# Kernel tuning notes

Measured on AMD Instinct MI355X. Metric: run time of the kernel, lower is better.

## Reference

```python
import jax, jax.numpy as jnp
import numpy as np

N_EMBED = 256
N_HEAD = 8
HEAD = N_EMBED // N_HEAD
LN_EPS = 1e-5


def _layernorm(x, g, b):
    mu = jnp.mean(x, axis=-1, keepdims=True)
    var = jnp.mean(jnp.square(x - mu), axis=-1, keepdims=True)
    return (x - mu) * jax.lax.rsqrt(var + LN_EPS) * g + b


def setup_inputs() -> dict:
    key = jax.random.key(0)
    ks = jax.random.split(key, 12)
    B, T, C, H, D = 16, 1024, N_EMBED, N_HEAD, HEAD
    s = C ** -0.5
    return {
        "x": jax.random.normal(ks[0], (B, T, C), jnp.float32),
        "wq": jax.random.normal(ks[1], (H, C, D), jnp.float32) * s,
        "wk": jax.random.normal(ks[2], (H, C, D), jnp.float32) * s,
        "wv": jax.random.normal(ks[3], (H, C, D), jnp.float32) * s,
        "w_proj": jax.random.normal(ks[4], (C, C), jnp.float32) * s,
        "b_proj": jnp.zeros((C,), jnp.float32),
        "w1": jax.random.normal(ks[5], (C, 4 * C), jnp.float32) * s,
        "b1": jnp.zeros((4 * C,), jnp.float32),
        "w2": jax.random.normal(ks[6], (4 * C, C), jnp.float32) * (4 * C) ** -0.5,
        "b2": jnp.zeros((C,), jnp.float32),
        "ln1_g": jnp.ones((C,), jnp.float32),
        "ln1_b": jnp.zeros((C,), jnp.float32),
        "ln2_g": jnp.ones((C,), jnp.float32),
        "ln2_b": jnp.zeros((C,), jnp.float32),
    }


def reference(x, wq, wk, wv, w_proj, b_proj, w1, b1, w2, b2,
              ln1_g, ln1_b, ln2_g, ln2_b):
    B, T, C = x.shape
    # --- multi-head causal self-attention on ln1(x) ---
    h = _layernorm(x, ln1_g, ln1_b)
    q = jnp.einsum('btc,hcd->bhtd', h, wq)
    k = jnp.einsum('btc,hcd->bhtd', h, wk)
    v = jnp.einsum('btc,hcd->bhtd', h, wv)
    # NOTE: original scales by n_embed**-0.5 (C of input), not head_size
    wei = jnp.einsum('bhtd,bhsd->bhts', q, k) * (C ** -0.5)
    causal = jnp.tril(jnp.ones((T, T), bool))
    wei = jnp.where(causal, wei, -jnp.inf)
    wei = jax.nn.softmax(wei, axis=-1)
    att = jnp.einsum('bhts,bhsd->bhtd', wei, v)
    att = att.transpose(0, 2, 1, 3).reshape(B, T, C)  # concat heads
    x = x + att @ w_proj + b_proj
    # --- feedforward on ln2(x) ---
    h2 = _layernorm(x, ln2_g, ln2_b)
    f = jax.nn.relu(h2 @ w1 + b1) @ w2 + b2
    return x + f
```

## Files before the change

### kernel.cpp

```cpp
#include <hip/hip_runtime.h>


typedef unsigned short u16;
typedef unsigned int u32;
typedef __attribute__((ext_vector_type(8))) short short8v;
typedef __attribute__((ext_vector_type(4))) float float4v;

__device__ __forceinline__ float b2f(u16 u) { union { u32 i; float f; } v; v.i = (u32)u << 16; return v.f; }
__device__ __forceinline__ float lo2f(u32 u) { union { u32 i; float f; } v; v.i = u << 16; return v.f; }
__device__ __forceinline__ float hi2f(u32 u) { union { u32 i; float f; } v; v.i = u & 0xffff0000u; return v.f; }
__device__ __forceinline__ u16 f2b(float f) {
    union { float f; u32 i; } v; v.f = f;
    u32 r = v.i + 0x7fffu + ((v.i >> 16) & 1u);
    return (u16)(r >> 16);
}
__device__ __forceinline__ u32 pk2_rtz(float a, float b) {
    return (__float_as_uint(a) >> 16) | (__float_as_uint(b) & 0xffff0000u);
}
__device__ __forceinline__ void async_cp16(const u16* g, u16* l) {
    __builtin_amdgcn_global_load_lds((const __attribute__((address_space(1))) void*)g,
                                     (__attribute__((address_space(3))) void*)l, 16, 0, 0);
}

__global__ __launch_bounds__(256) void prep_ln1(const float* __restrict__ wq,
                                                const float* __restrict__ wk,
                                                const float* __restrict__ wv,
                                                const float* __restrict__ wp,
                                                const float* __restrict__ w1,
                                                const float* __restrict__ w2,
                                                const float* __restrict__ x,
                                                const float* __restrict__ g1,
                                                const float* __restrict__ be1,
                                                u16* __restrict__ wqkvT,
                                                u16* __restrict__ wpT,
                                                u16* __restrict__ w1T,
                                                u16* __restrict__ w2T,
                                                u16* __restrict__ hout) {
    __shared__ u16 tile[64][65];
    int bid = blockIdx.x, tid = threadIdx.x;
    if (bid < 768) {
        int i = bid * 256 + tid;
        int n = i >> 8, k = i & 255;
        int which = n >> 8, nn = n & 255;
        const float* w = which == 0 ? wq : (which == 1 ? wk : wv);
        float v = w[((nn >> 5) * 256 + k) * 32 + (nn & 31)];
        if (which == 0) v *= 0.09016844f;
        wqkvT[i] = f2b(v);
    } else if (bid < 912) {
        const float* src; u16* dst; int K, N, t;
        if (bid < 784)      { src = wp; dst = wpT; K = 256;  N = 256;  t = bid - 768; }
        else if (bid < 848) { src = w1; dst = w1T; K = 256;  N = 1024; t = bid - 784; }
        else                { src = w2; dst = w2T; K = 1024; N = 256;  t = bid - 848; }
        int ntn = N >> 6;
        int k0 = (t / ntn) << 6, n0 = (t % ntn) << 6;
        int lane = tid & 63, wrow = tid >> 6;
        #pragma unroll
        for (int r = 0; r < 16; r++) {
            int k = wrow * 16 + r;
            tile[k][lane] = f2b(src[(size_t)(k0 + k) * N + n0 + lane]);
        }
        __syncthreads();
        #pragma unroll
        for (int r = 0; r < 16; r++) {
            int n = wrow * 16 + r;
            dst[(size_t)(n0 + n) * K + k0 + lane] = tile[lane][n];
        }
    } else {
        int row = (bid - 912) * 4 + (tid >> 6);
        int lane = tid & 63;
        float4 xv = *(const float4*)(x + (size_t)row * 256 + lane * 4);
        float v0 = xv.x, v1 = xv.y, v2 = xv.z, v3 = xv.w;
        float s = v0 + v1 + v2 + v3;
        #pragma unroll
        for (int m = 32; m; m >>= 1) s += __shfl_xor(s, m);
        float mu = s * 0.00390625f;
        float d0 = v0 - mu, d1 = v1 - mu, d2 = v2 - mu, d3 = v3 - mu;
        float ss = d0 * d0 + d1 * d1 + d2 * d2 + d3 * d3;
        #pragma unroll
        for (int m = 32; m; m >>= 1) ss += __shfl_xor(ss, m);
        float rs = rsqrtf(ss * 0.00390625f + 1e-5f);
        float4 g = *(const float4*)(g1 + lane * 4);
        float4 b = *(const float4*)(be1 + lane * 4);
        uint2 r;
        r.x = (u32)f2b(d0 * rs * g.x + b.x) | ((u32)f2b(d1 * rs * g.y + b.y) << 16);
        r.y = (u32)f2b(d2 * rs * g.z + b.z) | ((u32)f2b(d3 * rs * g.w + b.w) << 16);
        *(uint2*)(hout + (size_t)row * 256 + lane * 4) = r;
    }
}

template<bool HASBIAS, bool RELU, bool QKV>
__global__ __launch_bounds__(256) void gemm128(const u16* __restrict__ A,
                                               const u16* __restrict__ Bt,
                                               const float* __restrict__ bias,
                                               u16* __restrict__ out,
                                               u16* __restrict__ vout,
                                               int M, int N, int K) {
    __shared__ __align__(16) u16 SH[17408];
    u16* As = SH;
    u16* Bs = SH + 128 * 64;
    const int tid = threadIdx.x, lane = tid & 63, w = tid >> 6;
    const int m0 = blockIdx.x * 128, n0 = blockIdx.y * 128;
    const int wm = (w & 1) * 64, wn = (w >> 1) * 64;
    const int fm = lane & 15, q = lane >> 4;

    float4v acc[4][4];
    #pragma unroll
    for (int i = 0; i < 4; i++)
        #pragma unroll
        for (int j = 0; j < 4; j++) acc[i][j] = (float4v){0.f, 0.f, 0.f, 0.f};

    const int kset = ((lane & 7) ^ (lane >> 3)) * 8;
    const u16* Ag = A  + (size_t)(m0 + w * 32 + (lane >> 3)) * K + kset;
    const u16* Bg = Bt + (size_t)(n0 + w * 32 + (lane >> 3)) * K + kset;
    u16* Asw = As + (w * 32) * 64;
    u16* Bsw = Bs + (w * 32) * 64;

    const int sw = fm & 7;
    for (int k0 = 0; k0 < K; k0 += 64) {
        __syncthreads();
        #pragma unroll
        for (int c = 0; c < 4; c++) {
            async_cp16(Ag + (size_t)c * 8 * K + k0, Asw + c * 8 * 64);
            async_cp16(Bg + (size_t)c * 8 * K + k0, Bsw + c * 8 * 64);
        }
        __syncthreads();
        #pragma unroll
        for (int kk = 0; kk < 64; kk += 32) {
            const int slot = (((kk >> 3) + q) ^ sw) * 8;
            short8v af[4], bf[4];
            #pragma unroll
            for (int mi = 0; mi < 4; mi++)
                af[mi] = *(const short8v*)&As[(wm + mi * 16 + fm) * 64 + slot];
            #pragma unroll
            for (int ni = 0; ni < 4; ni++)
                bf[ni] = *(const short8v*)&Bs[(wn + ni * 16 + fm) * 64 + slot];
            #pragma unroll
            for (int mi = 0; mi < 4; mi++)
                #pragma unroll
                for (int ni = 0; ni < 4; ni++)
                    acc[mi][ni] = __builtin_amdgcn_mfma_f32_16x16x32_bf16(
                        bf[ni], af[mi], acc[mi][ni], 0, 0, 0);
        }
    }

    if (QKV && n0 >= 512) {
        __syncthreads();
        #pragma unroll
        for (int mi = 0; mi < 4; mi++) {
            int ml = wm + mi * 16 + fm;
            #pragma unroll
            for (int ni = 0; ni < 4; ni++) {
                int nl = wn + ni * 16 + q * 4;
                #pragma unroll
                for (int r = 0; r < 4; r++)
                    SH[(nl + r) * 136 + ml] = f2b(acc[mi][ni][r]);
            }
        }
        __syncthreads();
        int r = tid & 127, c = (tid >> 7) << 6;
        int hd = (n0 - 512) + r;
        int b = m0 >> 10, t0 = m0 & 1023;
        u16* dst = vout + (size_t)(b * 256 + hd) * 1024 + t0 + c;
        const u16* srcT = SH + r * 136 + c;
        #pragma unroll
        for (int i = 0; i < 8; i++)
            *(uint4*)(dst + i * 8) = *(const uint4*)(srcT + i * 8);
        return;
    }

    #pragma unroll
    for (int mi = 0; mi < 4; mi++) {
        int row = m0 + wm + mi * 16 + fm;
        #pragma unroll
        for (int ni = 0; ni < 4; ni++) {
            int nb = n0 + wn + ni * 16 + q * 4;
            float v0 = acc[mi][ni][0], v1 = acc[mi][ni][1],
                  v2 = acc[mi][ni][2], v3 = acc[mi][ni][3];
            if (HASBIAS) {
                float4 bv = *(const float4*)&bias[nb];
                v0 += bv.x; v1 += bv.y; v2 += bv.z; v3 += bv.w;
            }
            if (RELU) {
                v0 = fmaxf(v0, 0.f); v1 = fmaxf(v1, 0.f);
                v2 = fmaxf(v2, 0.f); v3 = fmaxf(v3, 0.f);
            }
            size_t idx = (size_t)row * N + nb;
            uint2 ov;
            ov.x = (u32)f2b(v0) | ((u32)f2b(v1) << 16);
            ov.y = (u32)f2b(v2) | ((u32)f2b(v3) << 16);
            *(uint2*)&out[idx] = ov;
        }
    }
}

#define FFN_COMPUTE(ABASE, BBASE, ACC)                                            \
    _Pragma("unroll")                                                             \
    for (int kk = 0; kk < 64; kk += 32) {                                         \
        const int slot = (((kk >> 3) + q) ^ sw) * 8;                              \
        short8v af[2], bf[4];                                                     \
        _Pragma("unroll")                                                         \
        for (int mi = 0; mi < 2; mi++)                                            \
            af[mi] = *(const short8v*)&(ABASE)[(wm + mi * 16 + fm) * 64 + slot];  \
        _Pragma("unroll")                                                         \
        for (int ni = 0; ni < 4; ni++)                                            \
            bf[ni] = *(const short8v*)&(BBASE)[(wn + ni * 16 + fm) * 64 + slot];  \
        _Pragma("unroll")                                                         \
        for (int mi = 0; mi < 2; mi++)                                            \
            _Pragma("unroll")                                                     \
            for (int ni = 0; ni < 4; ni++)                                        \
                ACC[mi][ni] = __builtin_amdgcn_mfma_f32_16x16x32_bf16(            \
                    bf[ni], af[mi], ACC[mi][ni], 0, 0, 0);                        \
    }

__global__ __launch_bounds__(512, 2) void ffn_fused(const u16* __restrict__ h2,
                                                    const u16* __restrict__ w1T,
                                                    const float* __restrict__ b1,
                                                    const u16* __restrict__ w2T,
                                                    const float* __restrict__ b2,
                                                    const u16* __restrict__ x2b,
                                                    float* __restrict__ out) {
    __shared__ __align__(16) u16 SH[65536];
    u16* As = SH;
    u16* Ms = SH + 16384;
    u16* Bs = SH + 32768;
    const int tid = threadIdx.x, lane = tid & 63, w = tid >> 6;
    const int m0 = blockIdx.x * 64;
    const int wm = (w & 1) * 32;
    const int wn = (w >> 1) * 64;
    const int fm = lane & 15, q = lane >> 4;
    const int sw = fm & 7;
    const int kset = ((lane & 7) ^ (lane >> 3)) * 8;
    const int rb = w * 8 + (lane >> 3);

    auto issueB = [&](int t, u16* dst) {
        const int n2 = t >> 3, k2 = t & 3;
        if (((t >> 2) & 1) == 0) {
            const u16* src = w1T + (size_t)(n2 * 256 + rb) * 256 + k2 * 64 + kset;
            #pragma unroll
            for (int c = 0; c < 4; c++)
                async_cp16(src + (size_t)c * 64 * 256, dst + c * 4096);
        } else {
            const u16* src = w2T + (size_t)rb * 1024 + n2 * 256 + k2 * 64 + kset;
            #pragma unroll
            for (int c = 0; c < 4; c++)
                async_cp16(src + (size_t)c * 64 * 1024, dst + c * 4096);
        }
    };

    const u16* Ag = h2 + (size_t)(m0 + rb) * 256 + kset;
    #pragma unroll
    for (int kc = 0; kc < 4; kc++)
        async_cp16(Ag + kc * 64, As + kc * 4096 + w * 512);
    issueB(0, Bs + w * 512);
    issueB(1, Bs + 16384 + w * 512);

    float4v acc1[2][4], acc2[2][4];
    #pragma unroll
    for (int i = 0; i < 2; i++)
        #pragma unroll
        for (int j = 0; j < 4; j++) acc2[i][j] = (float4v){0.f, 0.f, 0.f, 0.f};

    #pragma unroll 1
    for (int t = 0; t < 32; ++t) {
        const int nch = t >> 3, ph = (t >> 2) & 1, kc = t & 3;
        if (t == 31) asm volatile("s_waitcnt vmcnt(0)" ::: "memory");
        else         asm volatile("s_waitcnt vmcnt(4)" ::: "memory");
        __builtin_amdgcn_s_barrier();
        const u16* Bb = Bs + (t & 1) * 16384;
        if (ph == 0) {
            if (kc == 0) {
                #pragma unroll
                for (int i = 0; i < 2; i++)
                    #pragma unroll
                    for (int j = 0; j < 4; j++) acc1[i][j] = (float4v){0.f, 0.f, 0.f, 0.f};
            }
            const u16* Ab = As + kc * 4096;
            FFN_COMPUTE(Ab, Bb, acc1);
            if (kc == 3) {
                #pragma unroll
                for (int ni = 0; ni < 4; ni++) {
                    const int c2 = wn + ni * 16 + q * 4;
                    const int kcM = c2 >> 6, cc = c2 & 63;
                    float4 bv = *(const float4*)&b1[nch * 256 + c2];
                    #pragma unroll
                    for (int mi = 0; mi < 2; mi++) {
                        const int row = wm + mi * 16 + fm;
                        float v0 = fmaxf(acc1[mi][ni][0] + bv.x, 0.f);
                        float v1 = fmaxf(acc1[mi][ni][1] + bv.y, 0.f);
                        float v2 = fmaxf(acc1[mi][ni][2] + bv.z, 0.f);
                        float v3 = fmaxf(acc1[mi][ni][3] + bv.w, 0.f);
                        uint2 pp;
                        pp.x = (u32)f2b(v0) | ((u32)f2b(v1) << 16);
                        pp.y = (u32)f2b(v2) | ((u32)f2b(v3) << 16);
                        *(uint2*)&Ms[kcM * 4096 + row * 64 +
                                     (((cc >> 3) ^ (row & 7)) * 8) + (cc & 7)] = pp;
                    }
                }
            }
        } else {
            const u16* Ab = Ms + kc * 4096;
            FFN_COMPUTE(Ab, Bb, acc2);
        }
        asm volatile("s_waitcnt lgkmcnt(0)" ::: "memory");
        __builtin_amdgcn_s_barrier();
        if (t + 2 < 32)
            issueB(t + 2, Bs + (t & 1) * 16384 + w * 512);
    }

    #pragma unroll
    for (int mi = 0; mi < 2; mi++) {
        const int row = m0 + wm + mi * 16 + fm;
        #pragma unroll
        for (int ni = 0; ni < 4; ni++) {
            const int nb = wn + ni * 16 + q * 4;
            size_t idx = (size_t)row * 256 + nb;
            float4 bv = *(const float4*)&b2[nb];
            uint2 rv = *(const uint2*)&x2b[idx];
            float v0 = acc2[mi][ni][0] + bv.x + lo2f(rv.x);
            float v1 = acc2[mi][ni][1] + bv.y + hi2f(rv.x);
            float v2 = acc2[mi][ni][2] + bv.z + lo2f(rv.y);
            float v3 = acc2[mi][ni][3] + bv.w + hi2f(rv.y);
            *(float4*)&out[idx] = (float4){v0, v1, v2, v3};
        }
    }
}

__global__ __launch_bounds__(256) void proj_ln2(const u16* __restrict__ att,
                                                const u16* __restrict__ wpT,
                                                const float* __restrict__ bp,
                                                const float* __restrict__ x,
                                                const float* __restrict__ g2,
                                                const float* __restrict__ be2,
                                                u16* __restrict__ x2b,
                                                u16* __restrict__ h2) {
    __shared__ __align__(16) u16 As[32 * 64];
    __shared__ __align__(16) u16 Bs[256 * 64];
    __shared__ float gs[256], bs[256], bps[256];
    __shared__ float ps[4][16], pq[4][16];
    const int tid = threadIdx.x, lane = tid & 63, w = tid >> 6;
    const int m0 = blockIdx.x * 32;
    const int wm = (w & 1) * 16, wn = (w >> 1) * 128;
    const int fm = lane & 15, q = lane >> 4;

    gs[tid] = g2[tid]; bs[tid] = be2[tid]; bps[tid] = bp[tid];

    float4v acc[8];
    #pragma unroll
    for (int i = 0; i < 8; i++) acc[i] = (float4v){0.f, 0.f, 0.f, 0.f};

    const int kset = ((lane & 7) ^ (lane >> 3)) * 8;
    const u16* Ag = att + (size_t)(m0 + w * 8 + (lane >> 3)) * 256 + kset;
    const u16* Bg = wpT + (size_t)(w * 64 + (lane >> 3)) * 256 + kset;
    u16* Asw = As + (w * 8) * 64;
    u16* Bsw = Bs + (w * 64) * 64;

    const int sw = fm & 7;
    for (int k0 = 0; k0 < 256; k0 += 64) {
        __syncthreads();
        async_cp16(Ag + k0, Asw);
        #pragma unroll
        for (int c = 0; c < 8; c++)
            async_cp16(Bg + (size_t)c * 8 * 256 + k0, Bsw + c * 8 * 64);
        __syncthreads();
        #pragma unroll
        for (int kk = 0; kk < 64; kk += 32) {
            const int slot = (((kk >> 3) + q) ^ sw) * 8;
            short8v af = *(const short8v*)&As[(wm + fm) * 64 + slot];
            #pragma unroll
            for (int ni = 0; ni < 8; ni++) {
                short8v bf = *(const short8v*)&Bs[(wn + ni * 16 + fm) * 64 + slot];
                acc[ni] = __builtin_amdgcn_mfma_f32_16x16x32_bf16(bf, af, acc[ni], 0, 0, 0);
            }
        }
    }

    int m = m0 + wm + fm;
    float v[8][4];
    float s = 0.f, sq = 0.f;
    #pragma unroll
    for (int ni = 0; ni < 8; ni++) {
        int nb = wn + ni * 16 + q * 4;
        float4 xv = *(const float4*)(x + (size_t)m * 256 + nb);
        float4 bv = *(const float4*)&bps[nb];
        #pragma unroll
        for (int r = 0; r < 4; r++) {
            float t = acc[ni][r] + (&bv.x)[r] + (&xv.x)[r];
            v[ni][r] = t;
            s += t; sq += t * t;
        }
    }
    s += __shfl_xor(s, 16);  s += __shfl_xor(s, 32);
    sq += __shfl_xor(sq, 16); sq += __shfl_xor(sq, 32);
    if (q == 0) { ps[w][fm] = s; pq[w][fm] = sq; }
    __syncthreads();
    s = ps[w][fm] + ps[w ^ 2][fm];
    sq = pq[w][fm] + pq[w ^ 2][fm];
    float mu = s * 0.00390625f;
    float rs = rsqrtf(sq * 0.00390625f - mu * mu + 1e-5f);
    #pragma unroll
    for (int ni = 0; ni < 8; ni++) {
        int nb = wn + ni * 16 + q * 4;
        size_t idx = (size_t)m * 256 + nb;
        float4 gv = *(const float4*)&gs[nb];
        float4 bv = *(const float4*)&bs[nb];
        uint2 xo, ho;
        xo.x = (u32)f2b(v[ni][0]) | ((u32)f2b(v[ni][1]) << 16);
        xo.y = (u32)f2b(v[ni][2]) | ((u32)f2b(v[ni][3]) << 16);
        float h0 = (v[ni][0] - mu) * rs * gv.x + bv.x;
        float h1 = (v[ni][1] - mu) * rs * gv.y + bv.y;
        float h2v = (v[ni][2] - mu) * rs * gv.z + bv.z;
        float h3 = (v[ni][3] - mu) * rs * gv.w + bv.w;
        ho.x = (u32)f2b(h0) | ((u32)f2b(h1) << 16);
        ho.y = (u32)f2b(h2v) | ((u32)f2b(h3) << 16);
        *(uint2*)&x2b[idx] = xo;
        *(uint2*)&h2[idx] = ho;
    }
}

__global__ __launch_bounds__(256) void attn_mfma(const u16* __restrict__ qk,
                                                 const u16* __restrict__ vtg,
                                                 u16* __restrict__ att) {
    const int T = 1024;
    int jj = (blockIdx.x + (blockIdx.y >> 3)) & 7;
    int b = blockIdx.y >> 3, hh = blockIdx.y & 7;
    int tid = threadIdx.x;
    int lane = tid & 63, w = tid >> 6;
    int fm = lane & 15, q = lane >> 4;

    __shared__ __align__(16) u16 Ks[64][72];
    __shared__ __align__(16) u16 Vt[32][72];
    __shared__ __align__(16) u16 Pl[4][16][72];

    size_t base = (size_t)b * T * 512;
    const u16* kb = qk + base + 256 + hh * 32;
    const u16* vt = vtg + (size_t)((b * 8 + hh) * 32) * 1024;
    const int krow = tid >> 2, kcol = (tid & 3) * 8;
    const int vd = tid >> 3, vs = (tid & 7) * 8;

    int qa0 = jj * 64, qb0 = (15 - jj) * 64;
    int tqa = qa0 + w * 16 + fm, tqb = qb0 + w * 16 + fm;
    short8v qfa = *(const short8v*)(qk + base + (size_t)tqa * 512 + hh * 32 + q * 8);
    short8v qfb = *(const short8v*)(qk + base + (size_t)tqb * 512 + hh * 32 + q * 8);
    float4v oa0 = {0.f, 0.f, 0.f, 0.f}, oa1 = {0.f, 0.f, 0.f, 0.f};
    float4v ob0 = {0.f, 0.f, 0.f, 0.f}, ob1 = {0.f, 0.f, 0.f, 0.f};
    float la = 0.f, lb = 0.f;
    int wqa = qa0 + w * 16, wqb = qb0 + w * 16;
    int nIter = 16 - jj;

    uint4 kreg = *(const uint4*)(kb + (size_t)krow * 512 + kcol);
    uint4 vreg = *(const uint4*)(vt + (size_t)vd * 1024 + vs);

    for (int it = 0; it < nIter; ++it) {
        int s0 = it << 6;
        __syncthreads();
        *(uint4*)&Ks[krow][kcol] = kreg;
        *(uint4*)&Vt[vd][vs] = vreg;
        __syncthreads();
        if (it + 1 < nIter) {
            int ns0 = s0 + 64;
            kreg = *(const uint4*)(kb + (size_t)(ns0 + krow) * 512 + kcol);
            vreg = *(const uint4*)(vt + (size_t)vd * 1024 + ns0 + vs);
        }
        short8v kf0 = *(const short8v*)&Ks[fm][q * 8];
        short8v kf1 = *(const short8v*)&Ks[16 + fm][q * 8];
        short8v kf2 = *(const short8v*)&Ks[32 + fm][q * 8];
        short8v kf3 = *(const short8v*)&Ks[48 + fm][q * 8];
        short8v vf00 = *(const short8v*)&Vt[fm][q * 8];
        short8v vf01 = *(const short8v*)&Vt[fm][32 + q * 8];
        short8v vf10 = *(const short8v*)&Vt[16 + fm][q * 8];
        short8v vf11 = *(const short8v*)&Vt[16 + fm][32 + q * 8];
        float4v z = {0.f, 0.f, 0.f, 0.f};

        #pragma unroll
        for (int t2 = 0; t2 < 2; t2++) {
            int wq0 = t2 ? wqa : wqb;
            if (s0 >= wq0 + 16) continue;
            int tq = t2 ? tqa : tqb;
            short8v qf = t2 ? qfa : qfb;
            float4v s_0 = __builtin_amdgcn_mfma_f32_16x16x32_bf16(kf0, qf, z, 0, 0, 0);
            float4v s_1 = __builtin_amdgcn_mfma_f32_16x16x32_bf16(kf1, qf, z, 0, 0, 0);
            float4v s_2 = __builtin_amdgcn_mfma_f32_16x16x32_bf16(kf2, qf, z, 0, 0, 0);
            float4v s_3 = __builtin_amdgcn_mfma_f32_16x16x32_bf16(kf3, qf, z, 0, 0, 0);
            float p[16];
            #pragma unroll
            for (int r = 0; r < 4; r++) {
                p[r] = exp2f(s_0[r]); p[4 + r] = exp2f(s_1[r]);
                p[8 + r] = exp2f(s_2[r]); p[12 + r] = exp2f(s_3[r]);
            }
            if (s0 + 63 > wq0) {
                int sb = s0 + q * 4;
                #pragma unroll
                for (int c = 0; c < 4; c++)
                    #pragma unroll
                    for (int r = 0; r < 4; r++)
                        if (sb + c * 16 + r > tq) p[c * 4 + r] = 0.f;
            }
            float rsum = 0.f;
            #pragma unroll
            for (int i = 0; i < 16; i++) rsum += p[i];
            rsum += __shfl_xor(rsum, 16);
            rsum += __shfl_xor(rsum, 32);
            if (t2) la += rsum; else lb += rsum;

            #pragma unroll
            for (int c = 0; c < 4; c++) {
                uint2 pp;
                pp.x = pk2_rtz(p[c * 4 + 0], p[c * 4 + 1]);
                pp.y = pk2_rtz(p[c * 4 + 2], p[c * 4 + 3]);
                *(uint2*)&Pl[w][fm][c * 16 + q * 4] = pp;
            }
            short8v pf0 = *(const short8v*)&Pl[w][fm][q * 8];
            short8v pf1 = *(const short8v*)&Pl[w][fm][32 + q * 8];
            if (t2) {
                oa0 = __builtin_amdgcn_mfma_f32_16x16x32_bf16(vf00, pf0, oa0, 0, 0, 0);
                oa0 = __builtin_amdgcn_mfma_f32_16x16x32_bf16(vf01, pf1, oa0, 0, 0, 0);
                oa1 = __builtin_amdgcn_mfma_f32_16x16x32_bf16(vf10, pf0, oa1, 0, 0, 0);
                oa1 = __builtin_amdgcn_mfma_f32_16x16x32_bf16(vf11, pf1, oa1, 0, 0, 0);
            } else {
                ob0 = __builtin_amdgcn_mfma_f32_16x16x32_bf16(vf00, pf0, ob0, 0, 0, 0);
                ob0 = __builtin_amdgcn_mfma_f32_16x16x32_bf16(vf01, pf1, ob0, 0, 0, 0);
                ob1 = __builtin_amdgcn_mfma_f32_16x16x32_bf16(vf10, pf0, ob1, 0, 0, 0);
                ob1 = __builtin_amdgcn_mfma_f32_16x16x32_bf16(vf11, pf1, ob1, 0, 0, 0);
            }
        }
    }

    #pragma unroll
    for (int t2 = 0; t2 < 2; t2++) {
        float inv = 1.f / (t2 ? la : lb);
        float4v o0 = t2 ? oa0 : ob0, o1 = t2 ? oa1 : ob1;
        int tq = t2 ? tqa : tqb;
        uint2 r0, r1;
        r0.x = (u32)f2b(o0[0] * inv) | ((u32)f2b(o0[1] * inv) << 16);
        r0.y = (u32)f2b(o0[2] * inv) | ((u32)f2b(o0[3] * inv) << 16);
        r1.x = (u32)f2b(o1[0] * inv) | ((u32)f2b(o1[1] * inv) << 16);
        r1.y = (u32)f2b(o1[2] * inv) | ((u32)f2b(o1[3] * inv) << 16);
        size_t o = (size_t)(b * T + tq) * 256 + hh * 32;
        *(uint2*)(att + o + q * 4) = r0;
        *(uint2*)(att + o + 16 + q * 4) = r1;
    }
}

extern "C" void kernel_launch(void* const* d_in, const int* in_sizes, int n_in,
                              void* d_out, int out_size, void* d_ws, size_t ws_size,
                              hipStream_t stream) {
    const int BT = 16 * 1024;
    const float* x      = (const float*)d_in[0];
    const float* wq     = (const float*)d_in[1];
    const float* wk     = (const float*)d_in[2];
    const float* wv     = (const float*)d_in[3];
    const float* w_proj = (const float*)d_in[4];
    const float* b_proj = (const float*)d_in[5];
    const float* w1     = (const float*)d_in[6];
    const float* b1     = (const float*)d_in[7];
    const float* w2     = (const float*)d_in[8];
    const float* b2     = (const float*)d_in[9];
    const float* ln1_g  = (const float*)d_in[10];
    const float* ln1_b  = (const float*)d_in[11];
    const float* ln2_g  = (const float*)d_in[12];
    const float* ln2_b  = (const float*)d_in[13];

    char* ws = (char*)d_ws;
    const size_t MB = 1024 * 1024;
    u16*  x2b   = (u16*)(ws + 0);
    u16*  hbuf  = (u16*)(ws + 8 * MB);
    u16*  qk    = (u16*)(ws + 16 * MB);
    u16*  vtg   = (u16*)(ws + 32 * MB);
    u16*  wqkvT = (u16*)(ws + 48 * MB);
    u16*  wpT   = (u16*)(ws + 48 * MB + 0x60000);
    u16*  w1T   = (u16*)(ws + 48 * MB + 0x80000);
    u16*  w2T   = (u16*)(ws + 48 * MB + 0x100000);

    prep_ln1<<<5008, 256, 0, stream>>>(wq, wk, wv, w_proj, w1, w2, x, ln1_g, ln1_b,
                                       wqkvT, wpT, w1T, w2T, hbuf);
    gemm128<false, false, true><<<dim3(128, 6), 256, 0, stream>>>(
        hbuf, wqkvT, nullptr, qk, vtg, BT, 512, 256);
    attn_mfma<<<dim3(8, 128), 256, 0, stream>>>(qk, vtg, hbuf);
    proj_ln2<<<512, 256, 0, stream>>>(hbuf, wpT, b_proj, x, ln2_g, ln2_b, x2b, hbuf);
    ffn_fused<<<256, 512, 0, stream>>>(hbuf, w1T, b1, w2T, b2, x2b, (float*)d_out);
}
```

Measured before the change: 188.7 us.

## Keep FFN A-tile in registers and triple-buffer weight tiles with one barrier

The fused FFN kernel now loads its h2 row tile straight from global memory into registers, instead of staging it in LDS. The LDS space this frees is used to triple-buffer the weight tiles. Each weight prefetch is issued right after the single per-iteration barrier, which removes the second barrier and the trailing lgkmcnt wait. The 32-step loop is also fully unrolled. In exchange, register pressure rises sharply: about 64 extra VGPRs for the A fragments, under a 512-thread launch bound, which risks spills or longer compile-time schedules.

```diff
diff --git a/kernel.cpp b/kernel.cpp
--- a/kernel.cpp
+++ b/kernel.cpp
@@ -193,25 +193,6 @@
     }
 }
 
-#define FFN_COMPUTE(ABASE, BBASE, ACC)                                            \
-    _Pragma("unroll")                                                             \
-    for (int kk = 0; kk < 64; kk += 32) {                                         \
-        const int slot = (((kk >> 3) + q) ^ sw) * 8;                              \
-        short8v af[2], bf[4];                                                     \
-        _Pragma("unroll")                                                         \
-        for (int mi = 0; mi < 2; mi++)                                            \
-            af[mi] = *(const short8v*)&(ABASE)[(wm + mi * 16 + fm) * 64 + slot];  \
-        _Pragma("unroll")                                                         \
-        for (int ni = 0; ni < 4; ni++)                                            \
-            bf[ni] = *(const short8v*)&(BBASE)[(wn + ni * 16 + fm) * 64 + slot];  \
-        _Pragma("unroll")                                                         \
-        for (int mi = 0; mi < 2; mi++)                                            \
-            _Pragma("unroll")                                                     \
-            for (int ni = 0; ni < 4; ni++)                                        \
-                ACC[mi][ni] = __builtin_amdgcn_mfma_f32_16x16x32_bf16(            \
-                    bf[ni], af[mi], ACC[mi][ni], 0, 0, 0);                        \
-    }
-
 __global__ __launch_bounds__(512, 2) void ffn_fused(const u16* __restrict__ h2,
                                                     const u16* __restrict__ w1T,
                                                     const float* __restrict__ b1,
@@ -220,9 +201,8 @@
                                                     const u16* __restrict__ x2b,
                                                     float* __restrict__ out) {
     __shared__ __align__(16) u16 SH[65536];
-    u16* As = SH;
-    u16* Ms = SH + 16384;
-    u16* Bs = SH + 32768;
+    u16* Ms = SH;
+    u16* Bs = SH + 16384;
     const int tid = threadIdx.x, lane = tid & 63, w = tid >> 6;
     const int m0 = blockIdx.x * 64;
     const int wm = (w & 1) * 32;
@@ -232,6 +212,16 @@
     const int kset = ((lane & 7) ^ (lane >> 3)) * 8;
     const int rb = w * 8 + (lane >> 3);
 
+    short8v ar[8][2];
+    {
+        const u16* Abase = h2 + (size_t)(m0 + wm + fm) * 256 + q * 8;
+        #pragma unroll
+        for (int kcn = 0; kcn < 8; kcn++)
+            #pragma unroll
+            for (int mi = 0; mi < 2; mi++)
+                ar[kcn][mi] = *(const short8v*)(Abase + (size_t)mi * 16 * 256 + kcn * 32);
+    }
+
     auto issueB = [&](int t, u16* dst) {
         const int n2 = t >> 3, k2 = t & 3;
         if (((t >> 2) & 1) == 0) {
@@ -247,10 +237,6 @@
         }
     };
 
-    const u16* Ag = h2 + (size_t)(m0 + rb) * 256 + kset;
-    #pragma unroll
-    for (int kc = 0; kc < 4; kc++)
-        async_cp16(Ag + kc * 64, As + kc * 4096 + w * 512);
     issueB(0, Bs + w * 512);
     issueB(1, Bs + 16384 + w * 512);
 
@@ -260,13 +246,15 @@
         #pragma unroll
         for (int j = 0; j < 4; j++) acc2[i][j] = (float4v){0.f, 0.f, 0.f, 0.f};
 
-    #pragma unroll 1
+    #pragma unroll
     for (int t = 0; t < 32; ++t) {
         const int nch = t >> 3, ph = (t >> 2) & 1, kc = t & 3;
         if (t == 31) asm volatile("s_waitcnt vmcnt(0)" ::: "memory");
         else         asm volatile("s_waitcnt vmcnt(4)" ::: "memory");
         __builtin_amdgcn_s_barrier();
-        const u16* Bb = Bs + (t & 1) * 16384;
+        if (t + 2 < 32)
+            issueB(t + 2, Bs + ((t + 2) % 3) * 16384 + w * 512);
+        const u16* Bb = Bs + (t % 3) * 16384;
         if (ph == 0) {
             if (kc == 0) {
                 #pragma unroll
@@ -274,8 +262,20 @@
                     #pragma unroll
                     for (int j = 0; j < 4; j++) acc1[i][j] = (float4v){0.f, 0.f, 0.f, 0.f};
             }
-            const u16* Ab = As + kc * 4096;
-            FFN_COMPUTE(Ab, Bb, acc1);
+            #pragma unroll
+            for (int kk = 0; kk < 64; kk += 32) {
+                const int slot = (((kk >> 3) + q) ^ sw) * 8;
+                short8v bf[4];
+                #pragma unroll
+                for (int ni = 0; ni < 4; ni++)
+                    bf[ni] = *(const short8v*)&Bb[(wn + ni * 16 + fm) * 64 + slot];
+                #pragma unroll
+                for (int mi = 0; mi < 2; mi++)
+                    #pragma unroll
+                    for (int ni = 0; ni < 4; ni++)
+                        acc1[mi][ni] = __builtin_amdgcn_mfma_f32_16x16x32_bf16(
+                            bf[ni], ar[kc * 2 + (kk >> 5)][mi], acc1[mi][ni], 0, 0, 0);
+            }
             if (kc == 3) {
                 #pragma unroll
                 for (int ni = 0; ni < 4; ni++) {
@@ -296,15 +296,28 @@
                                      (((cc >> 3) ^ (row & 7)) * 8) + (cc & 7)] = pp;
                     }
                 }
+                asm volatile("s_waitcnt lgkmcnt(0)" ::: "memory");
             }
         } else {
             const u16* Ab = Ms + kc * 4096;
-            FFN_COMPUTE(Ab, Bb, acc2);
-        }
-        asm volatile("s_waitcnt lgkmcnt(0)" ::: "memory");
-        __builtin_amdgcn_s_barrier();
-        if (t + 2 < 32)
-            issueB(t + 2, Bs + (t & 1) * 16384 + w * 512);
+            #pragma unroll
+            for (int kk = 0; kk < 64; kk += 32) {
+                const int slot = (((kk >> 3) + q) ^ sw) * 8;
+                short8v af[2], bf[4];
+                #pragma unroll
+                for (int mi = 0; mi < 2; mi++)
+                    af[mi] = *(const short8v*)&Ab[(wm + mi * 16 + fm) * 64 + slot];
+                #pragma unroll
+                for (int ni = 0; ni < 4; ni++)
+                    bf[ni] = *(const short8v*)&Bb[(wn + ni * 16 + fm) * 64 + slot];
+                #pragma unroll
+                for (int mi = 0; mi < 2; mi++)
+                    #pragma unroll
+                    for (int ni = 0; ni < 4; ni++)
+                        acc2[mi][ni] = __builtin_amdgcn_mfma_f32_16x16x32_bf16(
+                            bf[ni], af[mi], acc2[mi][ni], 0, 0, 0);
+            }
+        }
     }
 
     #pragma unroll
```

Result: faster. 178.7 us (-5.3%).
